# Kernel tuning notes

Measured on AMD Instinct MI355X. Metric: run time of the kernel, lower is better.

Reference implementation:

```python
import jax, jax.numpy as jnp
import numpy as np

# Each of the 16 real-valued binary logic ops is a polynomial
#   c0 + c1*a + c2*b + c3*a*b
# Rows correspond to op_idx 0..15 from bin_op().
_OP_COEFFS = np.array([
    [0.,  0.,  0.,  0.],   # 0: false
    [0.,  0.,  0.,  1.],   # 1: a*b
    [0.,  1.,  0., -1.],   # 2: a*(1-b)
    [0.,  1.,  0.,  0.],   # 3: a
    [0.,  0.,  1., -1.],   # 4: (1-a)*b
    [0.,  0.,  1.,  0.],   # 5: b
    [0.,  1.,  1., -2.],   # 6: xor
    [0.,  1.,  1., -1.],   # 7: or
    [1., -1., -1.,  1.],   # 8: nor
    [1., -1., -1.,  2.],   # 9: xnor
    [1.,  0., -1.,  0.],   # 10: not b
    [1.,  0., -1.,  1.],   # 11: b -> a
    [1., -1.,  0.,  0.],   # 12: not a
    [1., -1.,  0.,  1.],   # 13: a -> b
    [1.,  0.,  0., -1.],   # 14: nand
    [1.,  0.,  0.,  0.],   # 15: true
], dtype=np.float32)

BATCH, IN_DIM, OUT_DIM = 2048, 16384, 16384


def setup_inputs() -> dict:
    key = jax.random.key(0)
    k1, k2, k3, k4 = jax.random.split(key, 4)
    x = jax.random.uniform(k1, (BATCH, IN_DIM), dtype=jnp.float32)
    idx_a = jax.random.randint(k2, (OUT_DIM,), 0, IN_DIM, dtype=jnp.int32)
    idx_b = jax.random.randint(k3, (OUT_DIM,), 0, IN_DIM, dtype=jnp.int32)
    weights = jax.random.normal(k4, (OUT_DIM, 16), dtype=jnp.float32)
    return {"x": x, "idx_a": idx_a, "idx_b": idx_b, "weights": weights}


def reference(x, idx_a, idx_b, weights):
    # gate probabilities over the 16 ops, per output neuron: [out_dim, 16]
    probs = jax.nn.softmax(weights, axis=-1)
    # collapse the 16-way weighted combination into 4 polynomial coeffs
    coef = probs @ jnp.asarray(_OP_COEFFS, dtype=probs.dtype)  # [out_dim, 4]
    a = x[:, idx_a]  # [batch, out_dim]
    b = x[:, idx_b]  # [batch, out_dim]
    out = coef[:, 0] + coef[:, 1] * a + coef[:, 2] * b + coef[:, 3] * (a * b)
    return out
```

## Files before the change

### kernel.cpp

```cpp
#include <hip/hip_runtime.h>
#include <hip/hip_fp16.h>

#define IN_DIM  16384
#define OUT_DIM 16384
#define BATCH   2048
#define TPB     512
#define NBLK    (BATCH / 2)
#define ITS     (OUT_DIM / (TPB * 4))
#define CHK     (IN_DIM / (TPB * 8))

typedef float f32x4 __attribute__((ext_vector_type(4)));

struct h2x2 { __half2 ab, cd; };

__device__ __constant__ float OPC[16][4] = {
    {0.f, 0.f, 0.f, 0.f}, {0.f, 0.f, 0.f, 1.f}, {0.f, 1.f, 0.f, -1.f}, {0.f, 1.f, 0.f, 0.f},
    {0.f, 0.f, 1.f, -1.f}, {0.f, 0.f, 1.f, 0.f}, {0.f, 1.f, 1.f, -2.f}, {0.f, 1.f, 1.f, -1.f},
    {1.f, -1.f, -1.f, 1.f}, {1.f, -1.f, -1.f, 2.f}, {1.f, 0.f, -1.f, 0.f}, {1.f, 0.f, -1.f, 1.f},
    {1.f, -1.f, 0.f, 0.f}, {1.f, -1.f, 0.f, 1.f}, {1.f, 0.f, 0.f, -1.f}, {1.f, 0.f, 0.f, 0.f}};

__global__ __launch_bounds__(64) void prep_kernel(const float* __restrict__ w,
                                                  const int* __restrict__ ia,
                                                  const int* __restrict__ ib,
                                                  h2x2* __restrict__ coefh,
                                                  unsigned* __restrict__ packed) {
    int j = blockIdx.x * 64 + threadIdx.x;
    if (j >= OUT_DIM) return;

    const float4* wr = (const float4*)(w + (size_t)j * 16);
    float wv[16];
    float4 w0 = wr[0], w1 = wr[1], w2 = wr[2], w3 = wr[3];
    wv[0] = w0.x; wv[1] = w0.y; wv[2] = w0.z; wv[3] = w0.w;
    wv[4] = w1.x; wv[5] = w1.y; wv[6] = w1.z; wv[7] = w1.w;
    wv[8] = w2.x; wv[9] = w2.y; wv[10] = w2.z; wv[11] = w2.w;
    wv[12] = w3.x; wv[13] = w3.y; wv[14] = w3.z; wv[15] = w3.w;

    float m = wv[0];
#pragma unroll
    for (int k = 1; k < 16; ++k) m = fmaxf(m, wv[k]);
    float s = 0.f;
#pragma unroll
    for (int k = 0; k < 16; ++k) { wv[k] = expf(wv[k] - m); s += wv[k]; }
    float inv = 1.f / s;

    float c0 = 0.f, c1 = 0.f, c2 = 0.f, c3 = 0.f;
#pragma unroll
    for (int k = 0; k < 16; ++k) {
        float p = wv[k];
        c0 = fmaf(p, OPC[k][0], c0);
        c1 = fmaf(p, OPC[k][1], c1);
        c2 = fmaf(p, OPC[k][2], c2);
        c3 = fmaf(p, OPC[k][3], c3);
    }
    h2x2 c;
    c.ab = __floats2half2_rn(c0 * inv, c1 * inv);
    c.cd = __floats2half2_rn(c2 * inv, c3 * inv);
    coefh[j] = c;
    packed[j] = ((unsigned)ia[j] << 2) | ((unsigned)ib[j] << 18);
}

__device__ __forceinline__ unsigned pack2(float a, float b) {
    return __builtin_bit_cast(unsigned, __builtin_amdgcn_cvt_pkrtz(a, b));
}

__global__ __launch_bounds__(TPB, 2) void logic_kernel(const float* __restrict__ x,
                                                       const unsigned* __restrict__ packed,
                                                       const h2x2* __restrict__ coefh,
                                                       float* __restrict__ out) {
    __shared__ __half lds[2 * IN_DIM];

    const int tid = threadIdx.x;
    const size_t rowA = (size_t)blockIdx.x * 2;

    {
        const float4* sA = (const float4*)(x + rowA * IN_DIM);
        const float4* sB = (const float4*)(x + (rowA + 1) * IN_DIM);
        float4 a[2 * CHK], b[2 * CHK];
#pragma unroll
        for (int c = 0; c < CHK; ++c) {
            const int m = (c * TPB + tid) * 2;
            a[2 * c + 0] = sA[m + 0];
            a[2 * c + 1] = sA[m + 1];
            b[2 * c + 0] = sB[m + 0];
            b[2 * c + 1] = sB[m + 1];
        }
#pragma unroll
        for (int c = 0; c < CHK; ++c) {
            uint4 t0, t1;
            t0.x = pack2(a[2 * c].x, b[2 * c].x); t0.y = pack2(a[2 * c].y, b[2 * c].y);
            t0.z = pack2(a[2 * c].z, b[2 * c].z); t0.w = pack2(a[2 * c].w, b[2 * c].w);
            t1.x = pack2(a[2 * c + 1].x, b[2 * c + 1].x); t1.y = pack2(a[2 * c + 1].y, b[2 * c + 1].y);
            t1.z = pack2(a[2 * c + 1].z, b[2 * c + 1].z); t1.w = pack2(a[2 * c + 1].w, b[2 * c + 1].w);
            char* dst = (char*)lds + (size_t)(c * TPB + tid) * 32;
            *(uint4*)dst = t0;
            *(uint4*)(dst + 16) = t1;
        }
    }

    uint4 pi = *(const uint4*)(packed + tid * 4);
    h2x2 cA = coefh[tid * 4 + 0];
    h2x2 cB = coefh[tid * 4 + 1];
    h2x2 cC = coefh[tid * 4 + 2];
    h2x2 cD = coefh[tid * 4 + 3];

    __syncthreads();

    const char* bufc = (const char*)lds;
    float* outrA = out + rowA * IN_DIM;
    float* outrB = outrA + IN_DIM;

#pragma unroll
    for (int it = 0; it < ITS; ++it) {
        uint4 pin = pi;
        h2x2 nA = cA, nB = cB, nC = cC, nD = cD;
        if (it + 1 < ITS) {
            const int jn = ((it + 1) * TPB + tid) * 4;
            pin = *(const uint4*)(packed + jn);
            nA = coefh[jn + 0];
            nB = coefh[jn + 1];
            nC = coefh[jn + 2];
            nD = coefh[jn + 3];
        }
        __builtin_amdgcn_sched_barrier(0);

        const int j0 = (it * TPB + tid) * 4;
        f32x4 oA, oB;
#define COL(P, CF, FLD)                                                              \
        {                                                                            \
            __half2 ap = *(const __half2*)(bufc + ((P) & 0xFFFFu));                  \
            __half2 bp = *(const __half2*)(bufc + ((P) >> 16));                      \
            float aA = __low2float(ap), aB = __high2float(ap);                       \
            float bA = __low2float(bp), bB = __high2float(bp);                       \
            float c0 = __low2float(CF.ab), c1 = __high2float(CF.ab);                 \
            float c2 = __low2float(CF.cd), c3 = __high2float(CF.cd);                 \
            oA.FLD = fmaf(aA, fmaf(c3, bA, c1), fmaf(c2, bA, c0));                   \
            oB.FLD = fmaf(aB, fmaf(c3, bB, c1), fmaf(c2, bB, c0));                   \
        }
        COL(pi.x, cA, x)
        COL(pi.y, cB, y)
        COL(pi.z, cC, z)
        COL(pi.w, cD, w)
#undef COL
        __builtin_nontemporal_store(oA, (f32x4*)(outrA + j0));
        __builtin_nontemporal_store(oB, (f32x4*)(outrB + j0));

        pi = pin; cA = nA; cB = nB; cC = nC; cD = nD;
    }
}

extern "C" void kernel_launch(void* const* d_in, const int* in_sizes, int n_in,
                              void* d_out, int out_size, void* d_ws, size_t ws_size,
                              hipStream_t stream) {
    const float* x = (const float*)d_in[0];
    const int* ia = (const int*)d_in[1];
    const int* ib = (const int*)d_in[2];
    const float* w = (const float*)d_in[3];
    float* out = (float*)d_out;

    h2x2* coefh = (h2x2*)d_ws;
    unsigned* packed = (unsigned*)((char*)d_ws + (size_t)OUT_DIM * sizeof(h2x2));

    prep_kernel<<<OUT_DIM / 64, 64, 0, stream>>>(w, ia, ib, coefh, packed);
    logic_kernel<<<NBLK, TPB, 0, stream>>>(x, packed, coefh, out);
}
```

Measured before the change: 48.77 us.

## Process four batch rows per block with interleaved fp16 LDS layout

Each block now stages four rows of x into LDS as interleaved halves (8 bytes per input column), so one 64-bit LDS gather serves four output rows and the index and coefficient loads are amortised over twice as many rows. The packed index encoding drops its byte-offset shift and the address is scaled by 8 at use. LDS per block doubles to 128 KB, occupancy drops to one block per CU, and the grid halves, which may reduce latency hiding during the load phase.

```diff
diff --git a/kernel.cpp b/kernel.cpp
--- a/kernel.cpp
+++ b/kernel.cpp
@@ -5,7 +5,7 @@
 #define OUT_DIM 16384
 #define BATCH   2048
 #define TPB     512
-#define NBLK    (BATCH / 2)
+#define NBLK    (BATCH / 4)
 #define ITS     (OUT_DIM / (TPB * 4))
 #define CHK     (IN_DIM / (TPB * 8))
 
@@ -56,44 +56,48 @@
     c.ab = __floats2half2_rn(c0 * inv, c1 * inv);
     c.cd = __floats2half2_rn(c2 * inv, c3 * inv);
     coefh[j] = c;
-    packed[j] = ((unsigned)ia[j] << 2) | ((unsigned)ib[j] << 18);
+    packed[j] = (unsigned)ia[j] | ((unsigned)ib[j] << 16);
 }
 
 __device__ __forceinline__ unsigned pack2(float a, float b) {
     return __builtin_bit_cast(unsigned, __builtin_amdgcn_cvt_pkrtz(a, b));
 }
 
-__global__ __launch_bounds__(TPB, 2) void logic_kernel(const float* __restrict__ x,
+__global__ __launch_bounds__(TPB, 1) void logic_kernel(const float* __restrict__ x,
                                                        const unsigned* __restrict__ packed,
                                                        const h2x2* __restrict__ coefh,
                                                        float* __restrict__ out) {
-    __shared__ __half lds[2 * IN_DIM];
+    __shared__ __half lds[4 * IN_DIM];
 
     const int tid = threadIdx.x;
-    const size_t rowA = (size_t)blockIdx.x * 2;
+    const size_t row0 = (size_t)blockIdx.x * 4;
 
     {
-        const float4* sA = (const float4*)(x + rowA * IN_DIM);
-        const float4* sB = (const float4*)(x + (rowA + 1) * IN_DIM);
-        float4 a[2 * CHK], b[2 * CHK];
+        const float4* s0 = (const float4*)(x + (row0 + 0) * IN_DIM);
+        const float4* s1 = (const float4*)(x + (row0 + 1) * IN_DIM);
+        const float4* s2 = (const float4*)(x + (row0 + 2) * IN_DIM);
+        const float4* s3 = (const float4*)(x + (row0 + 3) * IN_DIM);
 #pragma unroll
         for (int c = 0; c < CHK; ++c) {
             const int m = (c * TPB + tid) * 2;
-            a[2 * c + 0] = sA[m + 0];
-            a[2 * c + 1] = sA[m + 1];
-            b[2 * c + 0] = sB[m + 0];
-            b[2 * c + 1] = sB[m + 1];
-        }
-#pragma unroll
-        for (int c = 0; c < CHK; ++c) {
-            uint4 t0, t1;
-            t0.x = pack2(a[2 * c].x, b[2 * c].x); t0.y = pack2(a[2 * c].y, b[2 * c].y);
-            t0.z = pack2(a[2 * c].z, b[2 * c].z); t0.w = pack2(a[2 * c].w, b[2 * c].w);
-            t1.x = pack2(a[2 * c + 1].x, b[2 * c + 1].x); t1.y = pack2(a[2 * c + 1].y, b[2 * c + 1].y);
-            t1.z = pack2(a[2 * c + 1].z, b[2 * c + 1].z); t1.w = pack2(a[2 * c + 1].w, b[2 * c + 1].w);
-            char* dst = (char*)lds + (size_t)(c * TPB + tid) * 32;
-            *(uint4*)dst = t0;
+            float4 r0a = s0[m], r0b = s0[m + 1];
+            float4 r1a = s1[m], r1b = s1[m + 1];
+            float4 r2a = s2[m], r2b = s2[m + 1];
+            float4 r3a = s3[m], r3b = s3[m + 1];
+            uint4 t0, t1, t2, t3;
+            t0.x = pack2(r0a.x, r1a.x); t0.y = pack2(r2a.x, r3a.x);
+            t0.z = pack2(r0a.y, r1a.y); t0.w = pack2(r2a.y, r3a.y);
+            t1.x = pack2(r0a.z, r1a.z); t1.y = pack2(r2a.z, r3a.z);
+            t1.z = pack2(r0a.w, r1a.w); t1.w = pack2(r2a.w, r3a.w);
+            t2.x = pack2(r0b.x, r1b.x); t2.y = pack2(r2b.x, r3b.x);
+            t2.z = pack2(r0b.y, r1b.y); t2.w = pack2(r2b.y, r3b.y);
+            t3.x = pack2(r0b.z, r1b.z); t3.y = pack2(r2b.z, r3b.z);
+            t3.z = pack2(r0b.w, r1b.w); t3.w = pack2(r2b.w, r3b.w);
+            char* dst = (char*)lds + (size_t)(c * TPB + tid) * 64;
+            *(uint4*)(dst + 0)  = t0;
             *(uint4*)(dst + 16) = t1;
+            *(uint4*)(dst + 32) = t2;
+            *(uint4*)(dst + 48) = t3;
         }
     }
 
@@ -106,8 +110,10 @@
     __syncthreads();
 
     const char* bufc = (const char*)lds;
-    float* outrA = out + rowA * IN_DIM;
-    float* outrB = outrA + IN_DIM;
+    float* outr0 = out + row0 * IN_DIM;
+    float* outr1 = outr0 + IN_DIM;
+    float* outr2 = outr1 + IN_DIM;
+    float* outr3 = outr2 + IN_DIM;
 
 #pragma unroll
     for (int it = 0; it < ITS; ++it) {
@@ -124,25 +130,35 @@
         __builtin_amdgcn_sched_barrier(0);
 
         const int j0 = (it * TPB + tid) * 4;
-        f32x4 oA, oB;
+        f32x4 o0, o1, o2, o3;
 #define COL(P, CF, FLD)                                                              \
         {                                                                            \
-            __half2 ap = *(const __half2*)(bufc + ((P) & 0xFFFFu));                  \
-            __half2 bp = *(const __half2*)(bufc + ((P) >> 16));                      \
-            float aA = __low2float(ap), aB = __high2float(ap);                       \
-            float bA = __low2float(bp), bB = __high2float(bp);                       \
+            uint2 qa = *(const uint2*)(bufc + (size_t)((P) & 0xFFFFu) * 8);          \
+            uint2 qb = *(const uint2*)(bufc + (size_t)((P) >> 16) * 8);              \
+            __half2 a01 = __builtin_bit_cast(__half2, qa.x);                         \
+            __half2 a23 = __builtin_bit_cast(__half2, qa.y);                         \
+            __half2 b01 = __builtin_bit_cast(__half2, qb.x);                         \
+            __half2 b23 = __builtin_bit_cast(__half2, qb.y);                         \
             float c0 = __low2float(CF.ab), c1 = __high2float(CF.ab);                 \
             float c2 = __low2float(CF.cd), c3 = __high2float(CF.cd);                 \
-            oA.FLD = fmaf(aA, fmaf(c3, bA, c1), fmaf(c2, bA, c0));                   \
-            oB.FLD = fmaf(aB, fmaf(c3, bB, c1), fmaf(c2, bB, c0));                   \
+            float a0 = __low2float(a01), a1 = __high2float(a01);                     \
+            float a2 = __low2float(a23), a3 = __high2float(a23);                     \
+            float b0 = __low2float(b01), b1 = __high2float(b01);                     \
+            float b2 = __low2float(b23), b3 = __high2float(b23);                     \
+            o0.FLD = fmaf(a0, fmaf(c3, b0, c1), fmaf(c2, b0, c0));                   \
+            o1.FLD = fmaf(a1, fmaf(c3, b1, c1), fmaf(c2, b1, c0));                   \
+            o2.FLD = fmaf(a2, fmaf(c3, b2, c1), fmaf(c2, b2, c0));                   \
+            o3.FLD = fmaf(a3, fmaf(c3, b3, c1), fmaf(c2, b3, c0));                   \
         }
         COL(pi.x, cA, x)
         COL(pi.y, cB, y)
         COL(pi.z, cC, z)
         COL(pi.w, cD, w)
 #undef COL
-        __builtin_nontemporal_store(oA, (f32x4*)(outrA + j0));
-        __builtin_nontemporal_store(oB, (f32x4*)(outrB + j0));
+        __builtin_nontemporal_store(o0, (f32x4*)(outr0 + j0));
+        __builtin_nontemporal_store(o1, (f32x4*)(outr1 + j0));
+        __builtin_nontemporal_store(o2, (f32x4*)(outr2 + j0));
+        __builtin_nontemporal_store(o3, (f32x4*)(outr3 + j0));
 
         pi = pin; cA = nA; cB = nB; cC = nC; cD = nD;
     }
```

New measurement: 53.39 us. +9.5%, slower.
